# Kernel tuning notes

Measured on AMD Instinct MI355X. Metric: run time of the kernel, lower is better.

Reference implementation:

```python
import jax, jax.numpy as jnp
import numpy as np

N, B, H, OUT, T = 200000, 1024, 256, 128, 2  # nodes, graphs, hidden(=in_dim), out_dim, timesteps
NEG_SLOPE = 0.01


def setup_inputs() -> dict:
    key = jax.random.key(0)
    ks = jax.random.split(key, 12)
    s = 0.05
    f32 = jnp.float32
    return {
        "x": jax.random.normal(ks[0], (N, H), dtype=f32),
        "batch": jnp.sort(jax.random.randint(ks[1], (N,), 0, B)),
        # GATConv params (heads=1, shared lin for src/dst since in_channels is int)
        "W": jax.random.normal(ks[2], (H, H), dtype=f32) * s,
        "att_src": jax.random.normal(ks[3], (H,), dtype=f32) * s,
        "att_dst": jax.random.normal(ks[4], (H,), dtype=f32) * s,
        "bias_gat": jnp.zeros((H,), dtype=f32),
        # GRUCell params (input_size = H, hidden_size = H)
        "W_ih": jax.random.normal(ks[5], (3 * H, H), dtype=f32) * s,
        "W_hh": jax.random.normal(ks[6], (3 * H, H), dtype=f32) * s,
        "b_ih": jnp.zeros((3 * H,), dtype=f32),
        "b_hh": jnp.zeros((3 * H,), dtype=f32),
        # final Linear
        "W_lin": jax.random.normal(ks[7], (H, OUT), dtype=f32) * s,
        "b_lin": jnp.zeros((OUT,), dtype=f32),
    }


def reference(x, batch, W, att_src, att_dst, bias_gat, W_ih, W_hh, b_ih, b_hh, W_lin, b_lin):
    # out = global_add_pool(x, batch)  -> [B, H]
    out = jax.ops.segment_sum(x, batch, num_segments=B)
    for _ in range(T):
        # --- bipartite GATConv((x, out), edge_index=[arange(N), batch]) ---
        xs = x @ W                       # [N, H] transformed source nodes
        od = out @ W                     # [B, H] transformed dst (graph) nodes
        a_src = xs @ att_src             # [N]
        a_dst = od @ att_dst             # [B]
        e = a_src + a_dst[batch]         # [N] per-edge raw score (one edge per node)
        e = jnp.where(e > 0, e, NEG_SLOPE * e)  # leaky_relu(negative_slope=0.01)
        # scatter-softmax over each graph's incoming edges
        emax = jax.ops.segment_max(e, batch, num_segments=B)
        ee = jnp.exp(e - emax[batch])
        denom = jax.ops.segment_sum(ee, batch, num_segments=B)
        alpha = ee / denom[batch]        # [N]
        # scatter-add aggregation of weighted messages
        agg = jax.ops.segment_sum(xs * alpha[:, None], batch, num_segments=B) + bias_gat
        h = jax.nn.elu(agg)              # [B, H]  (dropout is identity in eval)
        # --- GRUCell(h, out) ---
        gi = h @ W_ih.T + b_ih           # [B, 3H]
        gh = out @ W_hh.T + b_hh         # [B, 3H]
        r = jax.nn.sigmoid(gi[:, :H] + gh[:, :H])
        z = jax.nn.sigmoid(gi[:, H:2 * H] + gh[:, H:2 * H])
        n = jnp.tanh(gi[:, 2 * H:] + r * gh[:, 2 * H:])
        out = jax.nn.silu((1.0 - z) * n + z * out)  # activation = F.silu
    return out @ W_lin + b_lin           # [B, OUT]
```

## Files before the change

kernel.cpp:

```cpp
#include <hip/hip_runtime.h>
#include <math.h>

#define N_NODES 200000
#define BGRAPH  1024
#define HDIM    256
#define ODIM    128
#define SCAP    1024

__global__ __launch_bounds__(256) void k_prep(const float* __restrict__ W,
        const float* __restrict__ att_src, const float* __restrict__ att_dst,
        const int* __restrict__ batch, float* __restrict__ v, float* __restrict__ u,
        int* __restrict__ seg) {
    int t = threadIdx.x;
    if (blockIdx.x < 256) {
        int i = blockIdx.x;
        float w = W[(size_t)i * HDIM + t];
        __shared__ float r1[256], r2[256];
        r1[t] = w * att_src[t];
        r2[t] = w * att_dst[t];
        __syncthreads();
        for (int st = 128; st > 0; st >>= 1) {
            if (t < st) { r1[t] += r1[t + st]; r2[t] += r2[t + st]; }
            __syncthreads();
        }
        if (t == 0) { v[i] = r1[0]; u[i] = r2[0]; }
    } else {
        int b = (blockIdx.x - 256) * 256 + t;
        if (b > BGRAPH) return;
        if (b == BGRAPH) { seg[b] = N_NODES; return; }
        int lo = 0, hi = N_NODES;
        while (lo < hi) { int mid = (lo + hi) >> 1; if (batch[mid] < b) lo = mid + 1; else hi = mid; }
        seg[b] = lo;
    }
}

__global__ __launch_bounds__(256) void k_passAB(const float* __restrict__ x,
        const int* __restrict__ seg, const float* __restrict__ v,
        const float* __restrict__ u, const float* __restrict__ W,
        const float* __restrict__ bias_gat,
        float* __restrict__ s, float* __restrict__ smax,
        float* __restrict__ stt, float* __restrict__ hbuf) {
    int b = blockIdx.x;
    int lo = seg[b], hi = seg[b + 1];
    int t = threadIdx.x, wave = t >> 6, lane = t & 63;
    float v0 = v[4 * lane + 0], v1 = v[4 * lane + 1], v2 = v[4 * lane + 2], v3 = v[4 * lane + 3];
    __shared__ float s_loc[SCAP];
    __shared__ float comb[4][HDIM];
    __shared__ float red[256];
    __shared__ float sred[4], dred[4];
    bool inl = (hi - lo) <= SCAP;

    float p0 = 0.f, p1 = 0.f, p2 = 0.f, p3 = 0.f;
    float sm = -3.402823466e38f;
    int i = lo + wave;
    for (; i + 4 < hi; i += 8) {
        const float4 r0 = *(const float4*)(x + (size_t)i * HDIM + 4 * lane);
        const float4 r1 = *(const float4*)(x + (size_t)(i + 4) * HDIM + 4 * lane);
        p0 += r0.x + r1.x; p1 += r0.y + r1.y; p2 += r0.z + r1.z; p3 += r0.w + r1.w;
        float pa = r0.x * v0 + r0.y * v1 + r0.z * v2 + r0.w * v3;
        float pb = r1.x * v0 + r1.y * v1 + r1.z * v2 + r1.w * v3;
        #pragma unroll
        for (int off = 32; off > 0; off >>= 1) {
            pa += __shfl_down(pa, off, 64);
            pb += __shfl_down(pb, off, 64);
        }
        if (lane == 0) {
            s[i] = pa; s[i + 4] = pb;
            if (inl) { s_loc[i - lo] = pa; s_loc[i + 4 - lo] = pb; }
            sm = fmaxf(sm, fmaxf(pa, pb));
        }
    }
    for (; i < hi; i += 4) {
        const float4 r0 = *(const float4*)(x + (size_t)i * HDIM + 4 * lane);
        p0 += r0.x; p1 += r0.y; p2 += r0.z; p3 += r0.w;
        float pa = r0.x * v0 + r0.y * v1 + r0.z * v2 + r0.w * v3;
        #pragma unroll
        for (int off = 32; off > 0; off >>= 1) pa += __shfl_down(pa, off, 64);
        if (lane == 0) {
            s[i] = pa;
            if (inl) s_loc[i - lo] = pa;
            sm = fmaxf(sm, pa);
        }
    }
    comb[wave][4 * lane + 0] = p0; comb[wave][4 * lane + 1] = p1;
    comb[wave][4 * lane + 2] = p2; comb[wave][4 * lane + 3] = p3;
    if (lane == 0) sred[wave] = sm;
    __syncthreads();
    float st0 = comb[0][t] + comb[1][t] + comb[2][t] + comb[3][t];
    stt[(size_t)b * HDIM + t] = st0;
    float smx = fmaxf(fmaxf(sred[0], sred[1]), fmaxf(sred[2], sred[3]));
    if (t == 0) smax[b] = smx;
    red[t] = st0 * u[t];
    __syncthreads();
    for (int st = 128; st > 0; st >>= 1) { if (t < st) red[t] += red[t + st]; __syncthreads(); }
    float d1 = red[0];
    __syncthreads();
    float M = smx + d1;
    M = M > 0.f ? M : 0.01f * M;

    float a0 = 0.f, a1 = 0.f, a2 = 0.f, a3 = 0.f, den = 0.f;
    i = lo + wave;
    for (; i + 4 < hi; i += 8) {
        float s0v = inl ? s_loc[i - lo]     : s[i];
        float s1v = inl ? s_loc[i + 4 - lo] : s[i + 4];
        float e0 = s0v + d1; e0 = e0 > 0.f ? e0 : 0.01f * e0;
        float e1 = s1v + d1; e1 = e1 > 0.f ? e1 : 0.01f * e1;
        float w0 = __expf(e0 - M), w1 = __expf(e1 - M);
        const float4 r0 = *(const float4*)(x + (size_t)i * HDIM + 4 * lane);
        const float4 r1 = *(const float4*)(x + (size_t)(i + 4) * HDIM + 4 * lane);
        den += w0 + w1;
        a0 += w0 * r0.x + w1 * r1.x; a1 += w0 * r0.y + w1 * r1.y;
        a2 += w0 * r0.z + w1 * r1.z; a3 += w0 * r0.w + w1 * r1.w;
    }
    for (; i < hi; i += 4) {
        float s0v = inl ? s_loc[i - lo] : s[i];
        float e0 = s0v + d1; e0 = e0 > 0.f ? e0 : 0.01f * e0;
        float w0 = __expf(e0 - M);
        const float4 r0 = *(const float4*)(x + (size_t)i * HDIM + 4 * lane);
        den += w0;
        a0 += w0 * r0.x; a1 += w0 * r0.y; a2 += w0 * r0.z; a3 += w0 * r0.w;
    }
    __syncthreads();
    comb[wave][4 * lane + 0] = a0; comb[wave][4 * lane + 1] = a1;
    comb[wave][4 * lane + 2] = a2; comb[wave][4 * lane + 3] = a3;
    if (lane == 0) dred[wave] = den;
    __syncthreads();
    float dtot = dred[0] + dred[1] + dred[2] + dred[3];
    float inv = (hi > lo) ? 1.0f / dtot : 0.f;
    __shared__ float ax[HDIM];
    ax[t] = (comb[0][t] + comb[1][t] + comb[2][t] + comb[3][t]) * inv;
    __syncthreads();
    float acc = bias_gat[t];
    #pragma unroll 8
    for (int ii = 0; ii < HDIM; ++ii) acc += ax[ii] * W[(size_t)ii * HDIM + t];
    hbuf[(size_t)b * HDIM + t] = acc > 0.f ? acc : expm1f(acc);
}

__global__ __launch_bounds__(256) void k_iter2(const float* __restrict__ x,
        const int* __restrict__ seg, const float* __restrict__ s,
        const float* __restrict__ u, const float* __restrict__ smax,
        float* __restrict__ stt,
        const float* __restrict__ gi, const float* __restrict__ gh,
        const float* __restrict__ b_ih, const float* __restrict__ b_hh,
        const float* __restrict__ W, const float* __restrict__ bias_gat,
        float* __restrict__ hbuf) {
    int b = blockIdx.x, t = threadIdx.x;
    int lo = seg[b], hi = seg[b + 1];
    size_t base = (size_t)b * (3 * HDIM);
    float gir = gi[base + t] + b_ih[t];
    float giz = gi[base + HDIM + t] + b_ih[HDIM + t];
    float gin = gi[base + 2 * HDIM + t] + b_ih[2 * HDIM + t];
    float ghr = gh[base + t] + b_hh[t];
    float ghz = gh[base + HDIM + t] + b_hh[HDIM + t];
    float ghn = gh[base + 2 * HDIM + t] + b_hh[2 * HDIM + t];
    float r = 1.f / (1.f + __expf(-(gir + ghr)));
    float z = 1.f / (1.f + __expf(-(giz + ghz)));
    float n = tanhf(gin + r * ghn);
    float prev = stt[(size_t)b * HDIM + t];
    float h2 = (1.f - z) * n + z * prev;
    float st_j = h2 / (1.f + __expf(-h2));
    stt[(size_t)b * HDIM + t] = st_j;

    __shared__ float red[256];
    red[t] = st_j * u[t];
    __syncthreads();
    for (int st = 128; st > 0; st >>= 1) { if (t < st) red[t] += red[t + st]; __syncthreads(); }
    float d2 = red[0];
    __syncthreads();
    float M = smax[b] + d2;
    M = M > 0.f ? M : 0.01f * M;

    int wave = t >> 6, lane = t & 63;
    float a0 = 0.f, a1 = 0.f, a2 = 0.f, a3 = 0.f, den = 0.f;
    int i = lo + wave;
    for (; i + 4 < hi; i += 8) {
        float e0 = s[i] + d2;     e0 = e0 > 0.f ? e0 : 0.01f * e0;
        float e1 = s[i + 4] + d2; e1 = e1 > 0.f ? e1 : 0.01f * e1;
        float w0 = __expf(e0 - M), w1 = __expf(e1 - M);
        const float4 r0 = *(const float4*)(x + (size_t)i * HDIM + 4 * lane);
        const float4 r1 = *(const float4*)(x + (size_t)(i + 4) * HDIM + 4 * lane);
        den += w0 + w1;
        a0 += w0 * r0.x + w1 * r1.x; a1 += w0 * r0.y + w1 * r1.y;
        a2 += w0 * r0.z + w1 * r1.z; a3 += w0 * r0.w + w1 * r1.w;
    }
    for (; i < hi; i += 4) {
        float e0 = s[i] + d2; e0 = e0 > 0.f ? e0 : 0.01f * e0;
        float w0 = __expf(e0 - M);
        const float4 r0 = *(const float4*)(x + (size_t)i * HDIM + 4 * lane);
        den += w0;
        a0 += w0 * r0.x; a1 += w0 * r0.y; a2 += w0 * r0.z; a3 += w0 * r0.w;
    }
    __shared__ float comb[4][HDIM];
    __shared__ float dred[4];
    comb[wave][4 * lane + 0] = a0; comb[wave][4 * lane + 1] = a1;
    comb[wave][4 * lane + 2] = a2; comb[wave][4 * lane + 3] = a3;
    if (lane == 0) dred[wave] = den;
    __syncthreads();
    float dtot = dred[0] + dred[1] + dred[2] + dred[3];
    float inv = (hi > lo) ? 1.0f / dtot : 0.f;
    __shared__ float ax[HDIM];
    ax[t] = (comb[0][t] + comb[1][t] + comb[2][t] + comb[3][t]) * inv;
    __syncthreads();
    float acc = bias_gat[t];
    #pragma unroll 8
    for (int ii = 0; ii < HDIM; ++ii) acc += ax[ii] * W[(size_t)ii * HDIM + t];
    hbuf[(size_t)b * HDIM + t] = acc > 0.f ? acc : expm1f(acc);
}

__global__ __launch_bounds__(256) void k_gemm2(const float* __restrict__ A0,
        const float* __restrict__ A1, const float* __restrict__ B0,
        const float* __restrict__ B1, float* __restrict__ C0, float* __restrict__ C1,
        int M, int N, int K) {
    const float* A = blockIdx.z ? A1 : A0;
    const float* B = blockIdx.z ? B1 : B0;
    float* C = blockIdx.z ? C1 : C0;
    __shared__ __align__(16) float As[16][64];
    __shared__ __align__(16) float Bs[16][64];
    int tx = threadIdx.x & 15, ty = threadIdx.x >> 4;
    int m0 = blockIdx.x * 64, n0 = blockIdx.y * 64;
    float acc[4][4] = {};
    for (int k0 = 0; k0 < K; k0 += 16) {
        {
            int r = threadIdx.x >> 2;
            int kk = (threadIdx.x & 3) << 2;
            float4 av = *(const float4*)(A + (size_t)(m0 + r) * K + k0 + kk);
            As[kk + 0][r] = av.x; As[kk + 1][r] = av.y;
            As[kk + 2][r] = av.z; As[kk + 3][r] = av.w;
            float4 bv = *(const float4*)(B + (size_t)(n0 + r) * K + k0 + kk);
            Bs[kk + 0][r] = bv.x; Bs[kk + 1][r] = bv.y;
            Bs[kk + 2][r] = bv.z; Bs[kk + 3][r] = bv.w;
        }
        __syncthreads();
        #pragma unroll
        for (int kk = 0; kk < 16; ++kk) {
            float4 a = *(const float4*)&As[kk][ty * 4];
            float4 bb = *(const float4*)&Bs[kk][tx * 4];
            acc[0][0] += a.x * bb.x; acc[0][1] += a.x * bb.y; acc[0][2] += a.x * bb.z; acc[0][3] += a.x * bb.w;
            acc[1][0] += a.y * bb.x; acc[1][1] += a.y * bb.y; acc[1][2] += a.y * bb.z; acc[1][3] += a.y * bb.w;
            acc[2][0] += a.z * bb.x; acc[2][1] += a.z * bb.y; acc[2][2] += a.z * bb.z; acc[2][3] += a.z * bb.w;
            acc[3][0] += a.w * bb.x; acc[3][1] += a.w * bb.y; acc[3][2] += a.w * bb.z; acc[3][3] += a.w * bb.w;
        }
        __syncthreads();
    }
    #pragma unroll
    for (int i = 0; i < 4; ++i) {
        int mrow = m0 + ty * 4 + i;
        *(float4*)(C + (size_t)mrow * N + n0 + tx * 4) =
            make_float4(acc[i][0], acc[i][1], acc[i][2], acc[i][3]);
    }
}

__global__ __launch_bounds__(256) void k_final(const float* __restrict__ gi,
        const float* __restrict__ gh, const float* __restrict__ b_ih,
        const float* __restrict__ b_hh, const float* __restrict__ stt,
        const float* __restrict__ B, const float* __restrict__ bias,
        float* __restrict__ C, int M, int N, int K) {
    __shared__ __align__(16) float As[16][64];
    __shared__ __align__(16) float Bs[16][64];
    int tx = threadIdx.x & 15, ty = threadIdx.x >> 4;
    int m0 = blockIdx.x * 64, n0 = blockIdx.y * 64;
    float acc[4][4] = {};
    for (int k0 = 0; k0 < K; k0 += 16) {
        {
            int r = threadIdx.x >> 2;
            int kk0 = (threadIdx.x & 3) << 2;
            int mrow = m0 + r;
            size_t base = (size_t)mrow * (3 * HDIM);
            #pragma unroll
            for (int q = 0; q < 4; ++q) {
                int k = k0 + kk0 + q;
                float gir = gi[base + k] + b_ih[k];
                float giz = gi[base + HDIM + k] + b_ih[HDIM + k];
                float gin = gi[base + 2 * HDIM + k] + b_ih[2 * HDIM + k];
                float ghr = gh[base + k] + b_hh[k];
                float ghz = gh[base + HDIM + k] + b_hh[HDIM + k];
                float ghn = gh[base + 2 * HDIM + k] + b_hh[2 * HDIM + k];
                float rg = 1.f / (1.f + __expf(-(gir + ghr)));
                float zg = 1.f / (1.f + __expf(-(giz + ghz)));
                float ng = tanhf(gin + rg * ghn);
                float prev = stt[(size_t)mrow * HDIM + k];
                float h2 = (1.f - zg) * ng + zg * prev;
                As[kk0 + q][r] = h2 / (1.f + __expf(-h2));
            }
        }
        {
            int kk = threadIdx.x >> 4;
            int nn = (threadIdx.x & 15) << 2;
            float4 bv = *(const float4*)(B + (size_t)(k0 + kk) * N + n0 + nn);
            Bs[kk][nn + 0] = bv.x; Bs[kk][nn + 1] = bv.y;
            Bs[kk][nn + 2] = bv.z; Bs[kk][nn + 3] = bv.w;
        }
        __syncthreads();
        #pragma unroll
        for (int kk = 0; kk < 16; ++kk) {
            float4 a = *(const float4*)&As[kk][ty * 4];
            float4 bb = *(const float4*)&Bs[kk][tx * 4];
            acc[0][0] += a.x * bb.x; acc[0][1] += a.x * bb.y; acc[0][2] += a.x * bb.z; acc[0][3] += a.x * bb.w;
            acc[1][0] += a.y * bb.x; acc[1][1] += a.y * bb.y; acc[1][2] += a.y * bb.z; acc[1][3] += a.y * bb.w;
            acc[2][0] += a.z * bb.x; acc[2][1] += a.z * bb.y; acc[2][2] += a.z * bb.z; acc[2][3] += a.z * bb.w;
            acc[3][0] += a.w * bb.x; acc[3][1] += a.w * bb.y; acc[3][2] += a.w * bb.z; acc[3][3] += a.w * bb.w;
        }
        __syncthreads();
    }
    float bsv[4];
    #pragma unroll
    for (int j = 0; j < 4; ++j) bsv[j] = bias[n0 + tx * 4 + j];
    #pragma unroll
    for (int i = 0; i < 4; ++i) {
        int mrow = m0 + ty * 4 + i;
        *(float4*)(C + (size_t)mrow * N + n0 + tx * 4) =
            make_float4(acc[i][0] + bsv[0], acc[i][1] + bsv[1],
                        acc[i][2] + bsv[2], acc[i][3] + bsv[3]);
    }
}

extern "C" void kernel_launch(void* const* d_in, const int* in_sizes, int n_in,
                              void* d_out, int out_size, void* d_ws, size_t ws_size,
                              hipStream_t stream) {
    const float* x        = (const float*)d_in[0];
    const int*   batch    = (const int*)d_in[1];
    const float* W        = (const float*)d_in[2];
    const float* att_src  = (const float*)d_in[3];
    const float* att_dst  = (const float*)d_in[4];
    const float* bias_gat = (const float*)d_in[5];
    const float* W_ih     = (const float*)d_in[6];
    const float* W_hh     = (const float*)d_in[7];
    const float* b_ih     = (const float*)d_in[8];
    const float* b_hh     = (const float*)d_in[9];
    const float* W_lin    = (const float*)d_in[10];
    const float* b_lin    = (const float*)d_in[11];

    char* ws = (char*)d_ws;
    size_t off = 0;
    auto alloc = [&](size_t bytes) {
        void* p = (void*)(ws + off);
        off += (bytes + 255) & ~(size_t)255;
        return p;
    };
    int*   seg  = (int*)alloc((BGRAPH + 1) * 4);
    float* vv   = (float*)alloc(HDIM * 4);
    float* uu   = (float*)alloc(HDIM * 4);
    float* smax = (float*)alloc(BGRAPH * 4);
    float* s    = (float*)alloc((size_t)N_NODES * 4);
    float* stt  = (float*)alloc((size_t)BGRAPH * HDIM * 4);
    float* hbuf = (float*)alloc((size_t)BGRAPH * HDIM * 4);
    float* gi   = (float*)alloc((size_t)BGRAPH * 3 * HDIM * 4);
    float* gh   = (float*)alloc((size_t)BGRAPH * 3 * HDIM * 4);

    hipLaunchKernelGGL(k_prep, dim3(261), dim3(256), 0, stream,
                       W, att_src, att_dst, batch, vv, uu, seg);
    hipLaunchKernelGGL(k_passAB, dim3(BGRAPH), dim3(256), 0, stream,
                       x, seg, vv, uu, W, bias_gat, s, smax, stt, hbuf);
    hipLaunchKernelGGL(k_gemm2, dim3(BGRAPH / 64, (3 * HDIM) / 64, 2), dim3(256), 0,
                       stream, hbuf, stt, W_ih, W_hh, gi, gh, BGRAPH, 3 * HDIM, HDIM);
    hipLaunchKernelGGL(k_iter2, dim3(BGRAPH), dim3(256), 0, stream,
                       x, seg, s, uu, smax, stt, gi, gh, b_ih, b_hh, W, bias_gat, hbuf);
    hipLaunchKernelGGL(k_gemm2, dim3(BGRAPH / 64, (3 * HDIM) / 64, 2), dim3(256), 0,
                       stream, hbuf, stt, W_ih, W_hh, gi, gh, BGRAPH, 3 * HDIM, HDIM);
    hipLaunchKernelGGL(k_final, dim3(BGRAPH / 64, ODIM / 64), dim3(256), 0, stream,
                       gi, gh, b_ih, b_hh, stt, W_lin, b_lin, (float*)d_out,
                       BGRAPH, ODIM, HDIM);
}
```

Baseline: 508.0 us.

## Use bf16 MFMA for GRU gate GEMMs and unroll aggregation loops 4x

```diff
diff --git a/kernel.cpp b/kernel.cpp
--- a/kernel.cpp
+++ b/kernel.cpp
@@ -6,6 +6,16 @@
 #define HDIM    256
 #define ODIM    128
 #define SCAP    1024
+
+typedef __attribute__((ext_vector_type(8))) short short8;
+typedef __attribute__((ext_vector_type(4))) float f32x4;
+
+__device__ __forceinline__ unsigned short f2bf(float f) {
+    union { float f; unsigned int i; } c; c.f = f;
+    unsigned int i = c.i;
+    unsigned int r = i + 0x7FFFu + ((i >> 16) & 1u);
+    return (unsigned short)(r >> 16);
+}
 
 __global__ __launch_bounds__(256) void k_prep(const float* __restrict__ W,
         const float* __restrict__ att_src, const float* __restrict__ att_dst,
@@ -100,17 +110,26 @@
 
     float a0 = 0.f, a1 = 0.f, a2 = 0.f, a3 = 0.f, den = 0.f;
     i = lo + wave;
-    for (; i + 4 < hi; i += 8) {
-        float s0v = inl ? s_loc[i - lo]     : s[i];
-        float s1v = inl ? s_loc[i + 4 - lo] : s[i + 4];
+    for (; i + 12 < hi; i += 16) {
+        float s0v = inl ? s_loc[i - lo]      : s[i];
+        float s1v = inl ? s_loc[i + 4 - lo]  : s[i + 4];
+        float s2v = inl ? s_loc[i + 8 - lo]  : s[i + 8];
+        float s3v = inl ? s_loc[i + 12 - lo] : s[i + 12];
         float e0 = s0v + d1; e0 = e0 > 0.f ? e0 : 0.01f * e0;
         float e1 = s1v + d1; e1 = e1 > 0.f ? e1 : 0.01f * e1;
+        float e2 = s2v + d1; e2 = e2 > 0.f ? e2 : 0.01f * e2;
+        float e3 = s3v + d1; e3 = e3 > 0.f ? e3 : 0.01f * e3;
         float w0 = __expf(e0 - M), w1 = __expf(e1 - M);
+        float w2 = __expf(e2 - M), w3 = __expf(e3 - M);
         const float4 r0 = *(const float4*)(x + (size_t)i * HDIM + 4 * lane);
         const float4 r1 = *(const float4*)(x + (size_t)(i + 4) * HDIM + 4 * lane);
-        den += w0 + w1;
-        a0 += w0 * r0.x + w1 * r1.x; a1 += w0 * r0.y + w1 * r1.y;
-        a2 += w0 * r0.z + w1 * r1.z; a3 += w0 * r0.w + w1 * r1.w;
+        const float4 r2 = *(const float4*)(x + (size_t)(i + 8) * HDIM + 4 * lane);
+        const float4 r3 = *(const float4*)(x + (size_t)(i + 12) * HDIM + 4 * lane);
+        den += (w0 + w1) + (w2 + w3);
+        a0 += w0 * r0.x + w1 * r1.x + w2 * r2.x + w3 * r3.x;
+        a1 += w0 * r0.y + w1 * r1.y + w2 * r2.y + w3 * r3.y;
+        a2 += w0 * r0.z + w1 * r1.z + w2 * r2.z + w3 * r3.z;
+        a3 += w0 * r0.w + w1 * r1.w + w2 * r2.w + w3 * r3.w;
     }
     for (; i < hi; i += 4) {
         float s0v = inl ? s_loc[i - lo] : s[i];
@@ -173,15 +192,22 @@
     int wave = t >> 6, lane = t & 63;
     float a0 = 0.f, a1 = 0.f, a2 = 0.f, a3 = 0.f, den = 0.f;
     int i = lo + wave;
-    for (; i + 4 < hi; i += 8) {
-        float e0 = s[i] + d2;     e0 = e0 > 0.f ? e0 : 0.01f * e0;
-        float e1 = s[i + 4] + d2; e1 = e1 > 0.f ? e1 : 0.01f * e1;
+    for (; i + 12 < hi; i += 16) {
+        float e0 = s[i] + d2;      e0 = e0 > 0.f ? e0 : 0.01f * e0;
+        float e1 = s[i + 4] + d2;  e1 = e1 > 0.f ? e1 : 0.01f * e1;
+        float e2 = s[i + 8] + d2;  e2 = e2 > 0.f ? e2 : 0.01f * e2;
+        float e3 = s[i + 12] + d2; e3 = e3 > 0.f ? e3 : 0.01f * e3;
         float w0 = __expf(e0 - M), w1 = __expf(e1 - M);
+        float w2 = __expf(e2 - M), w3 = __expf(e3 - M);
         const float4 r0 = *(const float4*)(x + (size_t)i * HDIM + 4 * lane);
         const float4 r1 = *(const float4*)(x + (size_t)(i + 4) * HDIM + 4 * lane);
-        den += w0 + w1;
-        a0 += w0 * r0.x + w1 * r1.x; a1 += w0 * r0.y + w1 * r1.y;
-        a2 += w0 * r0.z + w1 * r1.z; a3 += w0 * r0.w + w1 * r1.w;
+        const float4 r2 = *(const float4*)(x + (size_t)(i + 8) * HDIM + 4 * lane);
+        const float4 r3 = *(const float4*)(x + (size_t)(i + 12) * HDIM + 4 * lane);
+        den += (w0 + w1) + (w2 + w3);
+        a0 += w0 * r0.x + w1 * r1.x + w2 * r2.x + w3 * r3.x;
+        a1 += w0 * r0.y + w1 * r1.y + w2 * r2.y + w3 * r3.y;
+        a2 += w0 * r0.z + w1 * r1.z + w2 * r2.z + w3 * r3.z;
+        a3 += w0 * r0.w + w1 * r1.w + w2 * r2.w + w3 * r3.w;
     }
     for (; i < hi; i += 4) {
         float e0 = s[i] + d2; e0 = e0 > 0.f ? e0 : 0.01f * e0;
@@ -207,47 +233,53 @@
     hbuf[(size_t)b * HDIM + t] = acc > 0.f ? acc : expm1f(acc);
 }
 
-__global__ __launch_bounds__(256) void k_gemm2(const float* __restrict__ A0,
+__global__ __launch_bounds__(256) void k_gemm2m(const float* __restrict__ A0,
         const float* __restrict__ A1, const float* __restrict__ B0,
-        const float* __restrict__ B1, float* __restrict__ C0, float* __restrict__ C1,
-        int M, int N, int K) {
+        const float* __restrict__ B1, float* __restrict__ C0, float* __restrict__ C1) {
+    const int K = HDIM, N = 3 * HDIM;
     const float* A = blockIdx.z ? A1 : A0;
-    const float* B = blockIdx.z ? B1 : B0;
+    const float* Bm = blockIdx.z ? B1 : B0;
     float* C = blockIdx.z ? C1 : C0;
-    __shared__ __align__(16) float As[16][64];
-    __shared__ __align__(16) float Bs[16][64];
-    int tx = threadIdx.x & 15, ty = threadIdx.x >> 4;
     int m0 = blockIdx.x * 64, n0 = blockIdx.y * 64;
-    float acc[4][4] = {};
-    for (int k0 = 0; k0 < K; k0 += 16) {
-        {
-            int r = threadIdx.x >> 2;
-            int kk = (threadIdx.x & 3) << 2;
-            float4 av = *(const float4*)(A + (size_t)(m0 + r) * K + k0 + kk);
-            As[kk + 0][r] = av.x; As[kk + 1][r] = av.y;
-            As[kk + 2][r] = av.z; As[kk + 3][r] = av.w;
-            float4 bv = *(const float4*)(B + (size_t)(n0 + r) * K + k0 + kk);
-            Bs[kk + 0][r] = bv.x; Bs[kk + 1][r] = bv.y;
-            Bs[kk + 2][r] = bv.z; Bs[kk + 3][r] = bv.w;
-        }
-        __syncthreads();
-        #pragma unroll
-        for (int kk = 0; kk < 16; ++kk) {
-            float4 a = *(const float4*)&As[kk][ty * 4];
-            float4 bb = *(const float4*)&Bs[kk][tx * 4];
-            acc[0][0] += a.x * bb.x; acc[0][1] += a.x * bb.y; acc[0][2] += a.x * bb.z; acc[0][3] += a.x * bb.w;
-            acc[1][0] += a.y * bb.x; acc[1][1] += a.y * bb.y; acc[1][2] += a.y * bb.z; acc[1][3] += a.y * bb.w;
-            acc[2][0] += a.z * bb.x; acc[2][1] += a.z * bb.y; acc[2][2] += a.z * bb.z; acc[2][3] += a.z * bb.w;
-            acc[3][0] += a.w * bb.x; acc[3][1] += a.w * bb.y; acc[3][2] += a.w * bb.z; acc[3][3] += a.w * bb.w;
+    __shared__ __align__(16) unsigned short As[64][40];
+    __shared__ __align__(16) unsigned short Bs[64][40];
+    int t = threadIdx.x;
+    int wave = t >> 6, lane = t & 63;
+    int quad = lane >> 4, l16 = lane & 15;
+    f32x4 acc[4] = {};
+    for (int k0 = 0; k0 < K; k0 += 32) {
+        int r = t >> 2;
+        int kq = (t & 3) << 3;
+        float4 av0 = *(const float4*)(A + (size_t)(m0 + r) * K + k0 + kq);
+        float4 av1 = *(const float4*)(A + (size_t)(m0 + r) * K + k0 + kq + 4);
+        short8 pa;
+        pa[0] = (short)f2bf(av0.x); pa[1] = (short)f2bf(av0.y);
+        pa[2] = (short)f2bf(av0.z); pa[3] = (short)f2bf(av0.w);
+        pa[4] = (short)f2bf(av1.x); pa[5] = (short)f2bf(av1.y);
+        pa[6] = (short)f2bf(av1.z); pa[7] = (short)f2bf(av1.w);
+        *(short8*)&As[r][kq] = pa;
+        float4 bv0 = *(const float4*)(Bm + (size_t)(n0 + r) * K + k0 + kq);
+        float4 bv1 = *(const float4*)(Bm + (size_t)(n0 + r) * K + k0 + kq + 4);
+        short8 pb;
+        pb[0] = (short)f2bf(bv0.x); pb[1] = (short)f2bf(bv0.y);
+        pb[2] = (short)f2bf(bv0.z); pb[3] = (short)f2bf(bv0.w);
+        pb[4] = (short)f2bf(bv1.x); pb[5] = (short)f2bf(bv1.y);
+        pb[6] = (short)f2bf(bv1.z); pb[7] = (short)f2bf(bv1.w);
+        *(short8*)&Bs[r][kq] = pb;
+        __syncthreads();
+        short8 a = *(const short8*)&As[wave * 16 + l16][quad * 8];
+        #pragma unroll
+        for (int tn = 0; tn < 4; ++tn) {
+            short8 bfr = *(const short8*)&Bs[tn * 16 + l16][quad * 8];
+            acc[tn] = __builtin_amdgcn_mfma_f32_16x16x32_bf16(a, bfr, acc[tn], 0, 0, 0);
         }
         __syncthreads();
     }
     #pragma unroll
-    for (int i = 0; i < 4; ++i) {
-        int mrow = m0 + ty * 4 + i;
-        *(float4*)(C + (size_t)mrow * N + n0 + tx * 4) =
-            make_float4(acc[i][0], acc[i][1], acc[i][2], acc[i][3]);
-    }
+    for (int tn = 0; tn < 4; ++tn)
+        #pragma unroll
+        for (int rr = 0; rr < 4; ++rr)
+            C[(size_t)(m0 + wave * 16 + quad * 4 + rr) * N + n0 + tn * 16 + l16] = acc[tn][rr];
 }
 
 __global__ __launch_bounds__(256) void k_final(const float* __restrict__ gi,
@@ -351,12 +383,12 @@
                        W, att_src, att_dst, batch, vv, uu, seg);
     hipLaunchKernelGGL(k_passAB, dim3(BGRAPH), dim3(256), 0, stream,
                        x, seg, vv, uu, W, bias_gat, s, smax, stt, hbuf);
-    hipLaunchKernelGGL(k_gemm2, dim3(BGRAPH / 64, (3 * HDIM) / 64, 2), dim3(256), 0,
-                       stream, hbuf, stt, W_ih, W_hh, gi, gh, BGRAPH, 3 * HDIM, HDIM);
+    hipLaunchKernelGGL(k_gemm2m, dim3(BGRAPH / 64, (3 * HDIM) / 64, 2), dim3(256), 0,
+                       stream, hbuf, stt, W_ih, W_hh, gi, gh);
     hipLaunchKernelGGL(k_iter2, dim3(BGRAPH), dim3(256), 0, stream,
                        x, seg, s, uu, smax, stt, gi, gh, b_ih, b_hh, W, bias_gat, hbuf);
-    hipLaunchKernelGGL(k_gemm2, dim3(BGRAPH / 64, (3 * HDIM) / 64, 2), dim3(256), 0,
-                       stream, hbuf, stt, W_ih, W_hh, gi, gh, BGRAPH, 3 * HDIM, HDIM);
+    hipLaunchKernelGGL(k_gemm2m, dim3(BGRAPH / 64, (3 * HDIM) / 64, 2), dim3(256), 0,
+                       stream, hbuf, stt, W_ih, W_hh, gi, gh);
     hipLaunchKernelGGL(k_final, dim3(BGRAPH / 64, ODIM / 64), dim3(256), 0, stream,
                        gi, gh, b_ih, b_hh, stt, W_lin, b_lin, (float*)d_out,
                        BGRAPH, ODIM, HDIM);
```

Result: faster. 482.7 us (-5.0%).
